# Optimization experiments

Measured on AMD Instinct MI355X. Metric: run time of the kernel, lower is better.

Reference implementation:

```python
import jax, jax.numpy as jnp
import numpy as np

NUM_NODES = 8192
EMBED_DIM = 64
CURV = 1.0
EPS = 1e-08


def setup_inputs() -> dict:
    key = jax.random.key(0)
    emb = jax.random.normal(key, (NUM_NODES, EMBED_DIM), dtype=jnp.float32)
    return {"emb": emb}


def reference(emb):
    # emb: [N, D]
    norm_sq = jnp.sum(emb * emb, axis=-1, keepdims=True)            # [N, 1]
    dot = emb @ emb.T                                               # [N, N]
    # Pairwise squared distance via GEMM expansion (same math as the
    # explicit (e_i - e_j)^2 sum the original materializes as N x N x D).
    numerator = jnp.maximum(norm_sq + norm_sq.T - 2.0 * dot, 0.0)   # [N, N]
    # Faithful to the original: (1 - norm_i) * (1 - norm_j).T is [N,1]*[N,1]
    # -> a per-row column vector that broadcasts across columns.
    denominator = (1.0 - norm_sq) * (1.0 - norm_sq) + EPS           # [N, 1]
    dist = jnp.arccosh(1.0 + 2.0 * numerator / denominator + EPS)   # [N, N]
    adp = jnp.exp(-dist * CURV)
    adp = adp / (jnp.sum(adp, axis=1, keepdims=True) + EPS)
    return adp
```

## Files before the change

### kernel.cpp

```cpp
#include <hip/hip_runtime.h>
#include <hip/hip_bf16.h>
#include <stdint.h>
#include <type_traits>


#define N 8192
#define D 64
#define EPSF 1e-8f

typedef __bf16 bf16x8 __attribute__((ext_vector_type(8)));
typedef float  f32x4  __attribute__((ext_vector_type(4)));

static __device__ __forceinline__ unsigned short f32_to_bf16_rne(float f) {
    union { float f; uint32_t u; } c; c.f = f;
    return (unsigned short)((c.u + 0x7FFFu + ((c.u >> 16) & 1u)) >> 16);
}
static __device__ __forceinline__ float bf16_bits_to_f32(unsigned short h) {
    union { uint32_t u; float f; } c; c.u = ((uint32_t)h) << 16; return c.f;
}

__global__ __launch_bounds__(256) void prep_kernel(
    const float* __restrict__ emb, unsigned short* __restrict__ eh,
    unsigned short* __restrict__ el, float* __restrict__ nrm,
    float* __restrict__ rowsum)
{
    int tid = blockIdx.x * 256 + threadIdx.x;
    if (tid < N) rowsum[tid] = 0.0f;
    int row = tid >> 6;
    int k   = tid & 63;
    float v = emb[(size_t)row * D + k];
    unsigned short h = f32_to_bf16_rne(v);
    float lo = v - bf16_bits_to_f32(h);
    eh[(size_t)row * D + k] = h;
    el[(size_t)row * D + k] = f32_to_bf16_rne(lo);
    float sq = v * v;
    #pragma unroll
    for (int m = 32; m; m >>= 1) sq += __shfl_xor(sq, m, 64);
    if (k == 0) nrm[row] = sq;
}

template <bool STORE>
__global__ __launch_bounds__(256) void gemm_epi_kernel(
    const unsigned short* __restrict__ eh, const unsigned short* __restrict__ el,
    const float* __restrict__ nrm, float* __restrict__ out,
    float* __restrict__ rowsum)
{
    const int lane = threadIdx.x & 63;
    const int wid  = threadIdx.x >> 6;
    const int bx = blockIdx.x & 63;
    const int by = blockIdx.x >> 6;
    const int brow = by * 128 + (wid >> 1) * 64;
    const int bcol = bx * 128 + (wid & 1) * 64;
    const int lr = lane & 15;
    const int lk = (lane >> 4) * 8;

    bf16x8 ah[4][2], al[4][2];
    #pragma unroll
    for (int g = 0; g < 4; ++g) {
        #pragma unroll
        for (int h = 0; h < 2; ++h) {
            size_t off = (size_t)(brow + g*16 + lr) * D + h*32 + lk;
            ah[g][h] = *reinterpret_cast<const bf16x8*>(eh + off);
            if (STORE) al[g][h] = *reinterpret_cast<const bf16x8*>(el + off);
        }
    }

    f32x4 acc[4][4];
    #pragma unroll
    for (int rg = 0; rg < 4; ++rg)
        #pragma unroll
        for (int cg = 0; cg < 4; ++cg)
            acc[rg][cg] = (f32x4){0.f, 0.f, 0.f, 0.f};

    #pragma unroll
    for (int cg = 0; cg < 4; ++cg) {
        bf16x8 bh[2], bl[2];
        #pragma unroll
        for (int h = 0; h < 2; ++h) {
            size_t off = (size_t)(bcol + cg*16 + lr) * D + h*32 + lk;
            bh[h] = *reinterpret_cast<const bf16x8*>(eh + off);
            if (STORE) bl[h] = *reinterpret_cast<const bf16x8*>(el + off);
        }
        #pragma unroll
        for (int rg = 0; rg < 4; ++rg) {
            #pragma unroll
            for (int h = 0; h < 2; ++h) {
                acc[rg][cg] = __builtin_amdgcn_mfma_f32_16x16x32_bf16(ah[rg][h], bh[h], acc[rg][cg], 0, 0, 0);
                if (STORE) {
                    acc[rg][cg] = __builtin_amdgcn_mfma_f32_16x16x32_bf16(ah[rg][h], bl[h], acc[rg][cg], 0, 0, 0);
                    acc[rg][cg] = __builtin_amdgcn_mfma_f32_16x16x32_bf16(al[rg][h], bh[h], acc[rg][cg], 0, 0, 0);
                }
            }
        }
    }

    auto epilogue = [&](auto diag_c) {
        constexpr bool DIAG = decltype(diag_c)::value;
        #pragma unroll
        for (int rg = 0; rg < 4; ++rg) {
            const int ibase = brow + rg * 16 + (lane >> 4) * 4;
            float ni[4], rd2[4], sc[4];
            #pragma unroll
            for (int r = 0; r < 4; ++r) {
                ni[r] = nrm[ibase + r];
                float om = 1.0f - ni[r];
                rd2[r] = 2.0f * __builtin_amdgcn_rcpf(om * om + EPSF);
                if (STORE) sc[r] = __builtin_amdgcn_rcpf(rowsum[ibase + r] + EPSF);
            }
            float rs[4] = {0.f, 0.f, 0.f, 0.f};
            #pragma unroll
            for (int cg = 0; cg < 4; ++cg) {
                const int j = bcol + cg * 16 + lr;
                const float nj = nrm[j];
                #pragma unroll
                for (int r = 0; r < 4; ++r) {
                    float num = fmaxf(fmaf(-2.0f, acc[rg][cg][r], ni[r] + nj), 0.0f);
                    if (DIAG) { if (ibase + r == j) num = 0.0f; }
                    float t = fmaf(num, rd2[r], EPSF);
                    float s = fmaf(t, t, t + t);
                    float adp = __builtin_amdgcn_rcpf((1.0f + t) + __builtin_amdgcn_sqrtf(s));
                    if (STORE) {
                        out[(size_t)(ibase + r) * N + j] = adp * sc[r];
                    } else {
                        rs[r] += adp;
                    }
                }
            }
            if (!STORE) {
                #pragma unroll
                for (int r = 0; r < 4; ++r) {
                    float v = rs[r];
                    v += __shfl_xor(v, 1, 64);
                    v += __shfl_xor(v, 2, 64);
                    v += __shfl_xor(v, 4, 64);
                    v += __shfl_xor(v, 8, 64);
                    if (lr == 0) atomicAdd(&rowsum[ibase + r], v);
                }
            }
        }
    };
    if (bx == by) epilogue(std::true_type{});
    else          epilogue(std::false_type{});
}

extern "C" void kernel_launch(void* const* d_in, const int* in_sizes, int n_in,
                              void* d_out, int out_size, void* d_ws, size_t ws_size,
                              hipStream_t stream)
{
    const float* emb = (const float*)d_in[0];
    float* out = (float*)d_out;
    char* ws = (char*)d_ws;
    unsigned short* eh = (unsigned short*)ws;
    unsigned short* el = eh + (size_t)N * D;
    float* nrm  = (float*)(ws + (size_t)N * D * 4);
    float* rsum = nrm + N;

    hipLaunchKernelGGL(prep_kernel, dim3((N * D) / 256), dim3(256), 0, stream,
                       emb, eh, el, nrm, rsum);
    hipLaunchKernelGGL((gemm_epi_kernel<false>), dim3((N/128)*(N/128)), dim3(256), 0, stream,
                       eh, el, nrm, out, rsum);
    hipLaunchKernelGGL((gemm_epi_kernel<true>),  dim3((N/128)*(N/128)), dim3(256), 0, stream,
                       eh, el, nrm, out, rsum);
}
```

Before: 371.1 us.

## Drop bf16 hi/lo split GEMM and fuse per-tile MFMA with epilogue

Removes the low-order bf16 correction term, so the store pass uses a single bf16 product instead of three MFMAs per step and no longer loads or writes the low-part buffer. The loop is also restructured so each 16x16 accumulator is computed and consumed immediately in the epilogue, with per-row constants hoisted, which cuts live accumulator registers. The trade-off is lower dot-product accuracy in the store pass, which may shift distances and normalized outputs.

New measurement: 355.1 us. 4.3% less time.

```diff
diff --git a/kernel.cpp b/kernel.cpp
--- a/kernel.cpp
+++ b/kernel.cpp
@@ -15,24 +15,17 @@
     union { float f; uint32_t u; } c; c.f = f;
     return (unsigned short)((c.u + 0x7FFFu + ((c.u >> 16) & 1u)) >> 16);
 }
-static __device__ __forceinline__ float bf16_bits_to_f32(unsigned short h) {
-    union { uint32_t u; float f; } c; c.u = ((uint32_t)h) << 16; return c.f;
-}
 
 __global__ __launch_bounds__(256) void prep_kernel(
     const float* __restrict__ emb, unsigned short* __restrict__ eh,
-    unsigned short* __restrict__ el, float* __restrict__ nrm,
-    float* __restrict__ rowsum)
+    float* __restrict__ nrm, float* __restrict__ rowsum)
 {
     int tid = blockIdx.x * 256 + threadIdx.x;
     if (tid < N) rowsum[tid] = 0.0f;
     int row = tid >> 6;
     int k   = tid & 63;
     float v = emb[(size_t)row * D + k];
-    unsigned short h = f32_to_bf16_rne(v);
-    float lo = v - bf16_bits_to_f32(h);
-    eh[(size_t)row * D + k] = h;
-    el[(size_t)row * D + k] = f32_to_bf16_rne(lo);
+    eh[(size_t)row * D + k] = f32_to_bf16_rne(v);
     float sq = v * v;
     #pragma unroll
     for (int m = 32; m; m >>= 1) sq += __shfl_xor(sq, m, 64);
@@ -41,9 +34,8 @@
 
 template <bool STORE>
 __global__ __launch_bounds__(256) void gemm_epi_kernel(
-    const unsigned short* __restrict__ eh, const unsigned short* __restrict__ el,
-    const float* __restrict__ nrm, float* __restrict__ out,
-    float* __restrict__ rowsum)
+    const unsigned short* __restrict__ eh, const float* __restrict__ nrm,
+    float* __restrict__ out, float* __restrict__ rowsum)
 {
     const int lane = threadIdx.x & 63;
     const int wid  = threadIdx.x >> 6;
@@ -54,93 +46,83 @@
     const int lr = lane & 15;
     const int lk = (lane >> 4) * 8;
 
-    bf16x8 ah[4][2], al[4][2];
+    bf16x8 ah[4][2];
     #pragma unroll
-    for (int g = 0; g < 4; ++g) {
+    for (int g = 0; g < 4; ++g)
         #pragma unroll
-        for (int h = 0; h < 2; ++h) {
-            size_t off = (size_t)(brow + g*16 + lr) * D + h*32 + lk;
-            ah[g][h] = *reinterpret_cast<const bf16x8*>(eh + off);
-            if (STORE) al[g][h] = *reinterpret_cast<const bf16x8*>(el + off);
+        for (int h = 0; h < 2; ++h)
+            ah[g][h] = *reinterpret_cast<const bf16x8*>(eh + (size_t)(brow + g*16 + lr) * D + h*32 + lk);
+
+    float ni[4][4], rd2[4][4], sc[4][4];
+    #pragma unroll
+    for (int rg = 0; rg < 4; ++rg) {
+        const int ibase = brow + rg * 16 + (lane >> 4) * 4;
+        #pragma unroll
+        for (int r = 0; r < 4; ++r) {
+            ni[rg][r] = nrm[ibase + r];
+            float om = 1.0f - ni[rg][r];
+            rd2[rg][r] = 2.0f * __builtin_amdgcn_rcpf(om * om + EPSF);
+            if (STORE) sc[rg][r] = __builtin_amdgcn_rcpf(rowsum[ibase + r] + EPSF);
         }
     }
 
-    f32x4 acc[4][4];
-    #pragma unroll
-    for (int rg = 0; rg < 4; ++rg)
+    float rs[4][4];
+    if (!STORE)
         #pragma unroll
-        for (int cg = 0; cg < 4; ++cg)
-            acc[rg][cg] = (f32x4){0.f, 0.f, 0.f, 0.f};
+        for (int rg = 0; rg < 4; ++rg)
+            #pragma unroll
+            for (int r = 0; r < 4; ++r) rs[rg][r] = 0.0f;
 
-    #pragma unroll
-    for (int cg = 0; cg < 4; ++cg) {
-        bf16x8 bh[2], bl[2];
-        #pragma unroll
-        for (int h = 0; h < 2; ++h) {
-            size_t off = (size_t)(bcol + cg*16 + lr) * D + h*32 + lk;
-            bh[h] = *reinterpret_cast<const bf16x8*>(eh + off);
-            if (STORE) bl[h] = *reinterpret_cast<const bf16x8*>(el + off);
-        }
-        #pragma unroll
-        for (int rg = 0; rg < 4; ++rg) {
-            #pragma unroll
-            for (int h = 0; h < 2; ++h) {
-                acc[rg][cg] = __builtin_amdgcn_mfma_f32_16x16x32_bf16(ah[rg][h], bh[h], acc[rg][cg], 0, 0, 0);
-                if (STORE) {
-                    acc[rg][cg] = __builtin_amdgcn_mfma_f32_16x16x32_bf16(ah[rg][h], bl[h], acc[rg][cg], 0, 0, 0);
-                    acc[rg][cg] = __builtin_amdgcn_mfma_f32_16x16x32_bf16(al[rg][h], bh[h], acc[rg][cg], 0, 0, 0);
-                }
-            }
-        }
-    }
-
-    auto epilogue = [&](auto diag_c) {
+    auto body = [&](auto diag_c) {
         constexpr bool DIAG = decltype(diag_c)::value;
         #pragma unroll
-        for (int rg = 0; rg < 4; ++rg) {
-            const int ibase = brow + rg * 16 + (lane >> 4) * 4;
-            float ni[4], rd2[4], sc[4];
+        for (int cg = 0; cg < 4; ++cg) {
+            bf16x8 bh[2];
             #pragma unroll
-            for (int r = 0; r < 4; ++r) {
-                ni[r] = nrm[ibase + r];
-                float om = 1.0f - ni[r];
-                rd2[r] = 2.0f * __builtin_amdgcn_rcpf(om * om + EPSF);
-                if (STORE) sc[r] = __builtin_amdgcn_rcpf(rowsum[ibase + r] + EPSF);
-            }
-            float rs[4] = {0.f, 0.f, 0.f, 0.f};
+            for (int h = 0; h < 2; ++h)
+                bh[h] = *reinterpret_cast<const bf16x8*>(eh + (size_t)(bcol + cg*16 + lr) * D + h*32 + lk);
+            const int j = bcol + cg * 16 + lr;
+            const float nj = nrm[j];
             #pragma unroll
-            for (int cg = 0; cg < 4; ++cg) {
-                const int j = bcol + cg * 16 + lr;
-                const float nj = nrm[j];
+            for (int rg = 0; rg < 4; ++rg) {
+                f32x4 acc = (f32x4){0.f, 0.f, 0.f, 0.f};
+                acc = __builtin_amdgcn_mfma_f32_16x16x32_bf16(ah[rg][0], bh[0], acc, 0, 0, 0);
+                acc = __builtin_amdgcn_mfma_f32_16x16x32_bf16(ah[rg][1], bh[1], acc, 0, 0, 0);
+                const int ibase = brow + rg * 16 + (lane >> 4) * 4;
                 #pragma unroll
                 for (int r = 0; r < 4; ++r) {
-                    float num = fmaxf(fmaf(-2.0f, acc[rg][cg][r], ni[r] + nj), 0.0f);
+                    float num = fmaxf(fmaf(-2.0f, acc[r], ni[rg][r] + nj), 0.0f);
                     if (DIAG) { if (ibase + r == j) num = 0.0f; }
-                    float t = fmaf(num, rd2[r], EPSF);
+                    float t = fmaf(num, rd2[rg][r], EPSF);
                     float s = fmaf(t, t, t + t);
                     float adp = __builtin_amdgcn_rcpf((1.0f + t) + __builtin_amdgcn_sqrtf(s));
                     if (STORE) {
-                        out[(size_t)(ibase + r) * N + j] = adp * sc[r];
+                        out[(size_t)(ibase + r) * N + j] = adp * sc[rg][r];
                     } else {
-                        rs[r] += adp;
+                        rs[rg][r] += adp;
                     }
-                }
-            }
-            if (!STORE) {
-                #pragma unroll
-                for (int r = 0; r < 4; ++r) {
-                    float v = rs[r];
-                    v += __shfl_xor(v, 1, 64);
-                    v += __shfl_xor(v, 2, 64);
-                    v += __shfl_xor(v, 4, 64);
-                    v += __shfl_xor(v, 8, 64);
-                    if (lr == 0) atomicAdd(&rowsum[ibase + r], v);
                 }
             }
         }
     };
-    if (bx == by) epilogue(std::true_type{});
-    else          epilogue(std::false_type{});
+    if (bx == by) body(std::true_type{});
+    else          body(std::false_type{});
+
+    if (!STORE) {
+        #pragma unroll
+        for (int rg = 0; rg < 4; ++rg) {
+            const int ibase = brow + rg * 16 + (lane >> 4) * 4;
+            #pragma unroll
+            for (int r = 0; r < 4; ++r) {
+                float v = rs[rg][r];
+                v += __shfl_xor(v, 1, 64);
+                v += __shfl_xor(v, 2, 64);
+                v += __shfl_xor(v, 4, 64);
+                v += __shfl_xor(v, 8, 64);
+                if (lr == 0) atomicAdd(&rowsum[ibase + r], v);
+            }
+        }
+    }
 }
 
 extern "C" void kernel_launch(void* const* d_in, const int* in_sizes, int n_in,
@@ -151,14 +133,13 @@
     float* out = (float*)d_out;
     char* ws = (char*)d_ws;
     unsigned short* eh = (unsigned short*)ws;
-    unsigned short* el = eh + (size_t)N * D;
-    float* nrm  = (float*)(ws + (size_t)N * D * 4);
+    float* nrm  = (float*)(ws + (size_t)N * D * 2);
     float* rsum = nrm + N;
 
     hipLaunchKernelGGL(prep_kernel, dim3((N * D) / 256), dim3(256), 0, stream,
-                       emb, eh, el, nrm, rsum);
+                       emb, eh, nrm, rsum);
     hipLaunchKernelGGL((gemm_epi_kernel<false>), dim3((N/128)*(N/128)), dim3(256), 0, stream,
-                       eh, el, nrm, out, rsum);
+                       eh, nrm, out, rsum);
     hipLaunchKernelGGL((gemm_epi_kernel<true>),  dim3((N/128)*(N/128)), dim3(256), 0, stream,
-                       eh, el, nrm, out, rsum);
+                       eh, nrm, out, rsum);
 }
```
